# Optimization experiments

Measured on AMD Instinct MI355X. Metric: run time of the kernel, lower is better.

The kernel has to match this reference:

```python
import jax, jax.numpy as jnp
import numpy as np

# Config values (from c.mean_shift / c.cuda in the original module)
EMBED_DIM = 32      # embedding_dim
BW = 2.0            # kernel_bandwidth
ETA = 0.5           # step_size
N_ITERS = 3         # nb_iterations
RES = 96            # pic_res (image is RES x RES, N = RES*RES pixels)


def setup_inputs() -> dict:
    key = jax.random.key(0)
    # Scale 0.1 keeps exp(BW * x^T x) well inside fp32 range, mimicking the
    # bounded embeddings produced by the upstream margin-loss-trained net.
    x_in = 0.1 * jax.random.normal(key, (1, EMBED_DIM, RES, RES), dtype=jnp.float32)
    return {"x_in": x_in}


def reference(x_in):
    # x_in: (1, D, RES, RES). One mean-shift step per iteration:
    #   K = exp(bw * X^T X)                      (N x N affinity)
    #   deg_j = sum_i K[i, j]                    (column degree; K is symmetric)
    #   X_new = eta * X @ (K / deg) + (1-eta) * X
    # (The original's torch.inverse(diag(deg)) is exactly 1/deg column scaling.)
    # All iterates are concatenated along dim 0, as in the torch code.
    res = x_in.shape[3]
    n = res * res
    xs = [x_in.reshape(EMBED_DIM, n)]
    for _ in range(N_ITERS):
        X = xs[-1]                                    # (D, N)
        K = jnp.exp(BW * jnp.einsum('di,dj->ij', X, X))  # (N, N)
        deg = K.sum(axis=0)                           # (N,) column sums
        xs.append(ETA * (X @ (K / deg)) + (1.0 - ETA) * X)
    # (N_ITERS+1, D, RES, RES)
    return jnp.stack(xs, axis=0).reshape(-1, EMBED_DIM, res, res)
```

## Files before the change

### kernel.cpp

```cpp
#include <hip/hip_runtime.h>
#include <hip/hip_bf16.h>


#define DIM 32
#define RESO 96
#define NPT (RESO * RESO)
#define NITER 3
#define ETA 0.5f
#define SCALE 2.88539008f

#define QB 128
#define NQB (NPT / QB)
#define KSEG 7
#define NCHUNK128 (NPT / 128)

typedef __bf16 bf16_t;
typedef __bf16 v8bf __attribute__((ext_vector_type(8)));
typedef float  v4f  __attribute__((ext_vector_type(4)));

__device__ __forceinline__ void gload_lds16(const bf16_t* g, bf16_t* l) {
    __builtin_amdgcn_global_load_lds(
        (const __attribute__((address_space(1))) void*)g,
        (__attribute__((address_space(3))) void*)l, 16, 0, 0);
}

__device__ __forceinline__ int keyinv(int m) {
    return ((m & 8) << 1) | ((m & 4) << 1) | ((m & 16) >> 2) | (m & 3);
}

__global__ __launch_bounds__(256, 4)
void pack_kernel(const float* __restrict__ X,
                 bf16_t* __restrict__ rows,
                 bf16_t* __restrict__ cols,
                 float* __restrict__ out_copy) {
    __shared__ float tt[32][33];
    const int tid = threadIdx.x;
    const int n0  = blockIdx.x * 32;
    const int inv = keyinv(tid & 31);

#pragma unroll
    for (int j = 0; j < 4; ++j) {
        int d = (tid >> 5) + j * 8;
        int n = tid & 31;
        float v = X[(size_t)d * NPT + n0 + n];
        tt[d][n] = v;
        cols[(size_t)d * NPT + n0 + inv] = (bf16_t)v;
        out_copy[(size_t)d * NPT + n0 + n] = v;
    }
    __syncthreads();

#pragma unroll
    for (int j = 0; j < 4; ++j) {
        int n = (tid >> 5) + j * 8;
        int d = tid & 31;
        rows[(size_t)(n0 + n) * DIM + d] = (bf16_t)tt[d][n];
    }
}

__global__ __launch_bounds__(512, 4)
void msattn_kernel(const float* __restrict__ Xcur,
                   const bf16_t* __restrict__ rows,
                   const bf16_t* __restrict__ cols,
                   float* __restrict__ part_num,
                   float* __restrict__ part_den) {
    __shared__ __align__(16) bf16_t tiles[2][8192];

    const int tid  = threadIdx.x;
    const int w    = tid >> 6;
    const int lane = tid & 63;
    const int quad = lane >> 4;
    const int l16  = lane & 15;
    const int qb   = blockIdx.x;
    const int ks   = blockIdx.y;
    const int c0   = (NCHUNK128 * ks) / KSEG;
    const int c1   = (NCHUNK128 * (ks + 1)) / KSEG;
    const int q0w  = qb * QB + w * 16;

    v8bf qfrag;
#pragma unroll
    for (int j = 0; j < 8; ++j) {
        float v = Xcur[(quad * 8 + j) * NPT + q0w + l16];
        qfrag[j] = (bf16_t)(v * SCALE);
    }

    v8bf ones;
#pragma unroll
    for (int j = 0; j < 8; ++j) ones[j] = (bf16_t)1.0f;

    const bf16_t* gsrc;
    int gdelta, hdelta, dstoff;
    if (w < 4) {
        gsrc = rows + ((size_t)c0 * 128 + w * 16 + l16) * DIM + quad * 8;
        gdelta = 128 * DIM;
        hdelta = 64 * DIM;
        dstoff = w * 512;
    } else {
        int r = w - 4, hh = r >> 1, g = r & 1;
        gsrc = cols + (size_t)(hh * 16 + l16) * NPT + c0 * 128 + g * 32 + quad * 8;
        gdelta = 128;
        hdelta = 64;
        dstoff = 2048 + (w - 4) * 512;
    }

    v4f acc0 = {0.f, 0.f, 0.f, 0.f};
    v4f acc1 = {0.f, 0.f, 0.f, 0.f};
    v4f dden = {0.f, 0.f, 0.f, 0.f};

    gload_lds16(gsrc,          &tiles[0][dstoff]);
    gload_lds16(gsrc + hdelta, &tiles[0][4096 + dstoff]);
    gsrc += gdelta;
    __syncthreads();

    for (int c = c0; c < c1; ++c) {
        const int cc = c - c0;
        const bf16_t* tb = tiles[cc & 1];

        if (c + 1 < c1) {
            bf16_t* nt = tiles[(cc + 1) & 1];
            gload_lds16(gsrc,          &nt[dstoff]);
            gload_lds16(gsrc + hdelta, &nt[4096 + dstoff]);
            gsrc += gdelta;
        }

#pragma unroll
        for (int h = 0; h < 2; ++h) {
            const bf16_t* th = tb + h * 4096;

            v4f s[4];
#pragma unroll
            for (int t = 0; t < 4; ++t) {
                v8bf ka = *(const v8bf*)&th[t * 512 + lane * 8];
                s[t] = __builtin_amdgcn_mfma_f32_16x16x32_bf16(ka, qfrag,
                           (v4f){0.f, 0.f, 0.f, 0.f}, 0, 0, 0);
            }

            v8bf b00 = *(const v8bf*)&th[2048 + 0 * 512 + lane * 8];
            v8bf b01 = *(const v8bf*)&th[2048 + 1 * 512 + lane * 8];
            v8bf b10 = *(const v8bf*)&th[2048 + 2 * 512 + lane * 8];
            v8bf b11 = *(const v8bf*)&th[2048 + 3 * 512 + lane * 8];

            v8bf pa0, pa1;
#pragma unroll
            for (int t = 0; t < 2; ++t)
#pragma unroll
                for (int r = 0; r < 4; ++r)
                    pa0[t * 4 + r] = (bf16_t)__builtin_amdgcn_exp2f(s[t][r]);
#pragma unroll
            for (int t = 0; t < 2; ++t)
#pragma unroll
                for (int r = 0; r < 4; ++r)
                    pa1[t * 4 + r] = (bf16_t)__builtin_amdgcn_exp2f(s[2 + t][r]);

            acc0 = __builtin_amdgcn_mfma_f32_16x16x32_bf16(pa0, b00, acc0, 0, 0, 0);
            acc1 = __builtin_amdgcn_mfma_f32_16x16x32_bf16(pa0, b10, acc1, 0, 0, 0);
            dden = __builtin_amdgcn_mfma_f32_16x16x32_bf16(pa0, ones, dden, 0, 0, 0);
            acc0 = __builtin_amdgcn_mfma_f32_16x16x32_bf16(pa1, b01, acc0, 0, 0, 0);
            acc1 = __builtin_amdgcn_mfma_f32_16x16x32_bf16(pa1, b11, acc1, 0, 0, 0);
            dden = __builtin_amdgcn_mfma_f32_16x16x32_bf16(pa1, ones, dden, 0, 0, 0);
        }

        __syncthreads();
    }

    float* pn = part_num + (size_t)ks * NPT * DIM;
#pragma unroll
    for (int r = 0; r < 4; ++r) {
        int gq = q0w + quad * 4 + r;
        pn[(size_t)gq * DIM + l16]      = acc0[r];
        pn[(size_t)gq * DIM + 16 + l16] = acc1[r];
    }
    if (l16 == 0) {
#pragma unroll
        for (int r = 0; r < 4; ++r)
            part_den[ks * NPT + q0w + quad * 4 + r] = dden[r];
    }
}

__global__ __launch_bounds__(512, 2)
void reduce_kernel(const float* __restrict__ part_num,
                   const float* __restrict__ part_den,
                   const float* __restrict__ Xcur,
                   float* __restrict__ Xnext,
                   bf16_t* __restrict__ rows_out,
                   bf16_t* __restrict__ cols_out) {
    __shared__ float tp[2][32][33];
    __shared__ float dpart[KSEG][32];
    __shared__ float txn[32][33];

    const int tid = threadIdx.x;
    const int q0  = blockIdx.x * 32;
    const int inv = keyinv(tid & 31);

    {
        int slot = tid & 255;
        int sh   = tid >> 8;
        int qq = slot >> 3, dq = slot & 7;
        const float* pb = &part_num[(size_t)(q0 + qq) * DIM + dq * 4];
        size_t seg = (size_t)NPT * DIM;
        int ssb = sh * 4;
        v4f s = *(const v4f*)&pb[(ssb + 0) * seg]
              + *(const v4f*)&pb[(ssb + 1) * seg]
              + *(const v4f*)&pb[(ssb + 2) * seg];
        if (sh == 0) s += *(const v4f*)&pb[3 * seg];
#pragma unroll
        for (int k = 0; k < 4; ++k) tp[sh][qq][dq * 4 + k] = s[k];
    }
    if (tid < KSEG * 32) {
        int ss = tid >> 5, q = tid & 31;
        dpart[ss][q] = part_den[ss * NPT + q0 + q];
    }
    __syncthreads();

#pragma unroll
    for (int e = 0; e < 2; ++e) {
        int idx = tid + e * 512;
        int d = idx >> 5, qq = idx & 31;
        float num = tp[0][qq][d] + tp[1][qq][d];
        float dn = dpart[0][qq] + dpart[1][qq] + dpart[2][qq] + dpart[3][qq]
                 + dpart[4][qq] + dpart[5][qq] + dpart[6][qq];
        float xo = Xcur[(size_t)d * NPT + q0 + qq];
        float xn = ETA * num / dn + (1.0f - ETA) * xo;
        Xnext[(size_t)d * NPT + q0 + qq] = xn;
        cols_out[(size_t)d * NPT + q0 + inv] = (bf16_t)xn;
        txn[qq][d] = xn;
    }
    __syncthreads();

#pragma unroll
    for (int e = 0; e < 2; ++e) {
        int idx = tid + e * 512;
        int qq = idx >> 5, d = idx & 31;
        rows_out[(size_t)(q0 + qq) * DIM + d] = (bf16_t)txn[qq][d];
    }
}

extern "C" void kernel_launch(void* const* d_in, const int* in_sizes, int n_in,
                              void* d_out, int out_size, void* d_ws, size_t ws_size,
                              hipStream_t stream) {
    const float* x_in = (const float*)d_in[0];
    float* out = (float*)d_out;

    const size_t DN = (size_t)DIM * NPT;
    bf16_t* rows0 = (bf16_t*)d_ws;
    bf16_t* cols0 = rows0 + DN;
    bf16_t* rows1 = cols0 + DN;
    bf16_t* cols1 = rows1 + DN;
    float* part_num = (float*)(cols1 + DN);
    float* part_den = part_num + (size_t)KSEG * NPT * DIM;

    pack_kernel<<<NPT / 32, 256, 0, stream>>>(x_in, rows0, cols0, out);

    for (int it = 0; it < NITER; ++it) {
        const float* Xcur = (it == 0) ? x_in : out + (size_t)it * DN;
        bf16_t* rin  = (it & 1) ? rows1 : rows0;
        bf16_t* cin  = (it & 1) ? cols1 : cols0;
        bf16_t* rout = (it & 1) ? rows0 : rows1;
        bf16_t* cout = (it & 1) ? cols0 : cols1;
        msattn_kernel<<<dim3(NQB, KSEG), 512, 0, stream>>>(Xcur, rin, cin,
                                                           part_num, part_den);
        reduce_kernel<<<NPT / 32, 512, 0, stream>>>(part_num, part_den, Xcur,
                                                    out + (size_t)(it + 1) * DN,
                                                    rout, cout);
    }
}
```

Before: 123.4 us.

## Keep 144 queries per block in registers and stream keys directly from global

The attention kernel now has each wave hold query fragments for 9 groups of 16 queries (144 per block) in registers. Each wave streams its own slice of keys and values straight from global memory with register double-buffering, replacing the LDS tile pipeline and the per-chunk block barriers. Per-wave partial sums are combined through LDS at the end. The key split drops from 7 to 4 segments, and a pre-scaled bf16 copy of the rows is produced in pack and reduce so the query load needs no conversion. The cost is much higher register pressure (occupancy bound lowered to 2), a cross-wave LDS reduction epilogue, and fewer blocks in the grid (64x4).

```diff
diff --git a/kernel.cpp b/kernel.cpp
--- a/kernel.cpp
+++ b/kernel.cpp
@@ -9,21 +9,17 @@
 #define ETA 0.5f
 #define SCALE 2.88539008f
 
-#define QB 128
+#define QB 144
 #define NQB (NPT / QB)
-#define KSEG 7
-#define NCHUNK128 (NPT / 128)
+#define NG 9
+#define KSEG 4
+#define CHUNK 256
+#define NCHUNK (NPT / CHUNK)
 
 typedef __bf16 bf16_t;
 typedef __bf16 v8bf __attribute__((ext_vector_type(8)));
 typedef float  v4f  __attribute__((ext_vector_type(4)));
 
-__device__ __forceinline__ void gload_lds16(const bf16_t* g, bf16_t* l) {
-    __builtin_amdgcn_global_load_lds(
-        (const __attribute__((address_space(1))) void*)g,
-        (__attribute__((address_space(3))) void*)l, 16, 0, 0);
-}
-
 __device__ __forceinline__ int keyinv(int m) {
     return ((m & 8) << 1) | ((m & 4) << 1) | ((m & 16) >> 2) | (m & 3);
 }
@@ -31,6 +27,7 @@
 __global__ __launch_bounds__(256, 4)
 void pack_kernel(const float* __restrict__ X,
                  bf16_t* __restrict__ rows,
+                 bf16_t* __restrict__ rows_s,
                  bf16_t* __restrict__ cols,
                  float* __restrict__ out_copy) {
     __shared__ float tt[32][33];
@@ -53,17 +50,20 @@
     for (int j = 0; j < 4; ++j) {
         int n = (tid >> 5) + j * 8;
         int d = tid & 31;
-        rows[(size_t)(n0 + n) * DIM + d] = (bf16_t)tt[d][n];
-    }
-}
-
-__global__ __launch_bounds__(512, 4)
-void msattn_kernel(const float* __restrict__ Xcur,
-                   const bf16_t* __restrict__ rows,
+        float v = tt[d][n];
+        rows[(size_t)(n0 + n) * DIM + d]   = (bf16_t)v;
+        rows_s[(size_t)(n0 + n) * DIM + d] = (bf16_t)(v * SCALE);
+    }
+}
+
+__global__ __launch_bounds__(512, 2)
+void msattn_kernel(const bf16_t* __restrict__ rows,
+                   const bf16_t* __restrict__ rows_s,
                    const bf16_t* __restrict__ cols,
                    float* __restrict__ part_num,
                    float* __restrict__ part_den) {
-    __shared__ __align__(16) bf16_t tiles[2][8192];
+    __shared__ float osum[8][48][33];
+    __shared__ float dsum[8][QB];
 
     const int tid  = threadIdx.x;
     const int w    = tid >> 6;
@@ -72,107 +72,105 @@
     const int l16  = lane & 15;
     const int qb   = blockIdx.x;
     const int ks   = blockIdx.y;
-    const int c0   = (NCHUNK128 * ks) / KSEG;
-    const int c1   = (NCHUNK128 * (ks + 1)) / KSEG;
-    const int q0w  = qb * QB + w * 16;
-
-    v8bf qfrag;
-#pragma unroll
-    for (int j = 0; j < 8; ++j) {
-        float v = Xcur[(quad * 8 + j) * NPT + q0w + l16];
-        qfrag[j] = (bf16_t)(v * SCALE);
-    }
+    const int c0   = ks * (NCHUNK / KSEG);
+    const int c1   = c0 + (NCHUNK / KSEG);
+    const int q0   = qb * QB;
+
+    v8bf qf[NG];
+#pragma unroll
+    for (int g = 0; g < NG; ++g)
+        qf[g] = *(const v8bf*)&rows_s[(size_t)(q0 + g * 16 + l16) * DIM + quad * 8];
 
     v8bf ones;
 #pragma unroll
     for (int j = 0; j < 8; ++j) ones[j] = (bf16_t)1.0f;
 
-    const bf16_t* gsrc;
-    int gdelta, hdelta, dstoff;
-    if (w < 4) {
-        gsrc = rows + ((size_t)c0 * 128 + w * 16 + l16) * DIM + quad * 8;
-        gdelta = 128 * DIM;
-        hdelta = 64 * DIM;
-        dstoff = w * 512;
-    } else {
-        int r = w - 4, hh = r >> 1, g = r & 1;
-        gsrc = cols + (size_t)(hh * 16 + l16) * NPT + c0 * 128 + g * 32 + quad * 8;
-        gdelta = 128;
-        hdelta = 64;
-        dstoff = 2048 + (w - 4) * 512;
-    }
-
-    v4f acc0 = {0.f, 0.f, 0.f, 0.f};
-    v4f acc1 = {0.f, 0.f, 0.f, 0.f};
-    v4f dden = {0.f, 0.f, 0.f, 0.f};
-
-    gload_lds16(gsrc,          &tiles[0][dstoff]);
-    gload_lds16(gsrc + hdelta, &tiles[0][4096 + dstoff]);
-    gsrc += gdelta;
-    __syncthreads();
+    const bf16_t* pA = rows + ((size_t)(c0 * CHUNK + w * 32 + l16)) * DIM + quad * 8;
+    const bf16_t* pB = cols + (size_t)l16 * NPT + c0 * CHUNK + w * 32 + quad * 8;
+
+    v4f acc[NG][2];
+    v4f den[NG];
+#pragma unroll
+    for (int g = 0; g < NG; ++g) {
+        acc[g][0] = (v4f){0.f, 0.f, 0.f, 0.f};
+        acc[g][1] = (v4f){0.f, 0.f, 0.f, 0.f};
+        den[g]    = (v4f){0.f, 0.f, 0.f, 0.f};
+    }
+
+    v8bf ka0 = *(const v8bf*)pA;
+    v8bf ka1 = *(const v8bf*)(pA + 16 * DIM);
+    v8bf bV0 = *(const v8bf*)pB;
+    v8bf bV1 = *(const v8bf*)(pB + (size_t)16 * NPT);
+    pA += CHUNK * DIM;
+    pB += CHUNK;
 
     for (int c = c0; c < c1; ++c) {
-        const int cc = c - c0;
-        const bf16_t* tb = tiles[cc & 1];
-
-        if (c + 1 < c1) {
-            bf16_t* nt = tiles[(cc + 1) & 1];
-            gload_lds16(gsrc,          &nt[dstoff]);
-            gload_lds16(gsrc + hdelta, &nt[4096 + dstoff]);
-            gsrc += gdelta;
-        }
-
-#pragma unroll
-        for (int h = 0; h < 2; ++h) {
-            const bf16_t* th = tb + h * 4096;
-
-            v4f s[4];
-#pragma unroll
-            for (int t = 0; t < 4; ++t) {
-                v8bf ka = *(const v8bf*)&th[t * 512 + lane * 8];
-                s[t] = __builtin_amdgcn_mfma_f32_16x16x32_bf16(ka, qfrag,
-                           (v4f){0.f, 0.f, 0.f, 0.f}, 0, 0, 0);
+        const bool more = (c + 1 < c1);
+        v8bf nka0, nka1, nb0, nb1;
+        if (more) {
+            nka0 = *(const v8bf*)pA;
+            nka1 = *(const v8bf*)(pA + 16 * DIM);
+            nb0  = *(const v8bf*)pB;
+            nb1  = *(const v8bf*)(pB + (size_t)16 * NPT);
+            pA += CHUNK * DIM;
+            pB += CHUNK;
+        }
+
+#pragma unroll
+        for (int g = 0; g < NG; ++g) {
+            v4f s0 = __builtin_amdgcn_mfma_f32_16x16x32_bf16(ka0, qf[g],
+                         (v4f){0.f, 0.f, 0.f, 0.f}, 0, 0, 0);
+            v4f s1 = __builtin_amdgcn_mfma_f32_16x16x32_bf16(ka1, qf[g],
+                         (v4f){0.f, 0.f, 0.f, 0.f}, 0, 0, 0);
+            v8bf pa;
+#pragma unroll
+            for (int r = 0; r < 4; ++r) {
+                pa[r]     = (bf16_t)__builtin_amdgcn_exp2f(s0[r]);
+                pa[4 + r] = (bf16_t)__builtin_amdgcn_exp2f(s1[r]);
             }
-
-            v8bf b00 = *(const v8bf*)&th[2048 + 0 * 512 + lane * 8];
-            v8bf b01 = *(const v8bf*)&th[2048 + 1 * 512 + lane * 8];
-            v8bf b10 = *(const v8bf*)&th[2048 + 2 * 512 + lane * 8];
-            v8bf b11 = *(const v8bf*)&th[2048 + 3 * 512 + lane * 8];
-
-            v8bf pa0, pa1;
-#pragma unroll
-            for (int t = 0; t < 2; ++t)
+            acc[g][0] = __builtin_amdgcn_mfma_f32_16x16x32_bf16(pa, bV0, acc[g][0], 0, 0, 0);
+            acc[g][1] = __builtin_amdgcn_mfma_f32_16x16x32_bf16(pa, bV1, acc[g][1], 0, 0, 0);
+            den[g]    = __builtin_amdgcn_mfma_f32_16x16x32_bf16(pa, ones, den[g], 0, 0, 0);
+        }
+
+        if (more) { ka0 = nka0; ka1 = nka1; bV0 = nb0; bV1 = nb1; }
+    }
+
+    if (l16 == 0) {
+#pragma unroll
+        for (int g = 0; g < NG; ++g)
+#pragma unroll
+            for (int r = 0; r < 4; ++r)
+                dsum[w][g * 16 + quad * 4 + r] = den[g][r];
+    }
+
+#pragma unroll
+    for (int round = 0; round < 3; ++round) {
+        if (round) __syncthreads();
+#pragma unroll
+        for (int gg = 0; gg < 3; ++gg) {
+            int g = round * 3 + gg;
+#pragma unroll
+            for (int h = 0; h < 2; ++h)
 #pragma unroll
                 for (int r = 0; r < 4; ++r)
-                    pa0[t * 4 + r] = (bf16_t)__builtin_amdgcn_exp2f(s[t][r]);
-#pragma unroll
-            for (int t = 0; t < 2; ++t)
-#pragma unroll
-                for (int r = 0; r < 4; ++r)
-                    pa1[t * 4 + r] = (bf16_t)__builtin_amdgcn_exp2f(s[2 + t][r]);
-
-            acc0 = __builtin_amdgcn_mfma_f32_16x16x32_bf16(pa0, b00, acc0, 0, 0, 0);
-            acc1 = __builtin_amdgcn_mfma_f32_16x16x32_bf16(pa0, b10, acc1, 0, 0, 0);
-            dden = __builtin_amdgcn_mfma_f32_16x16x32_bf16(pa0, ones, dden, 0, 0, 0);
-            acc0 = __builtin_amdgcn_mfma_f32_16x16x32_bf16(pa1, b01, acc0, 0, 0, 0);
-            acc1 = __builtin_amdgcn_mfma_f32_16x16x32_bf16(pa1, b11, acc1, 0, 0, 0);
-            dden = __builtin_amdgcn_mfma_f32_16x16x32_bf16(pa1, ones, dden, 0, 0, 0);
-        }
-
+                    osum[w][gg * 16 + quad * 4 + r][h * 16 + l16] = acc[g][h][r];
+        }
         __syncthreads();
-    }
-
-    float* pn = part_num + (size_t)ks * NPT * DIM;
-#pragma unroll
-    for (int r = 0; r < 4; ++r) {
-        int gq = q0w + quad * 4 + r;
-        pn[(size_t)gq * DIM + l16]      = acc0[r];
-        pn[(size_t)gq * DIM + 16 + l16] = acc1[r];
-    }
-    if (l16 == 0) {
-#pragma unroll
-        for (int r = 0; r < 4; ++r)
-            part_den[ks * NPT + q0w + quad * 4 + r] = dden[r];
+#pragma unroll
+        for (int e = 0; e < 3; ++e) {
+            int idx = tid + e * 512;
+            int qr = idx >> 5, d = idx & 31;
+            float s = osum[0][qr][d] + osum[1][qr][d] + osum[2][qr][d]
+                    + osum[3][qr][d] + osum[4][qr][d] + osum[5][qr][d]
+                    + osum[6][qr][d] + osum[7][qr][d];
+            part_num[((size_t)ks * NPT + q0 + round * 48 + qr) * DIM + d] = s;
+        }
+    }
+    if (tid < QB) {
+        float s = dsum[0][tid] + dsum[1][tid] + dsum[2][tid] + dsum[3][tid]
+                + dsum[4][tid] + dsum[5][tid] + dsum[6][tid] + dsum[7][tid];
+        part_den[ks * NPT + q0 + tid] = s;
     }
 }
 
@@ -182,6 +180,7 @@
                    const float* __restrict__ Xcur,
                    float* __restrict__ Xnext,
                    bf16_t* __restrict__ rows_out,
+                   bf16_t* __restrict__ rows_s_out,
                    bf16_t* __restrict__ cols_out) {
     __shared__ float tp[2][32][33];
     __shared__ float dpart[KSEG][32];
@@ -197,11 +196,8 @@
         int qq = slot >> 3, dq = slot & 7;
         const float* pb = &part_num[(size_t)(q0 + qq) * DIM + dq * 4];
         size_t seg = (size_t)NPT * DIM;
-        int ssb = sh * 4;
-        v4f s = *(const v4f*)&pb[(ssb + 0) * seg]
-              + *(const v4f*)&pb[(ssb + 1) * seg]
-              + *(const v4f*)&pb[(ssb + 2) * seg];
-        if (sh == 0) s += *(const v4f*)&pb[3 * seg];
+        v4f s = *(const v4f*)&pb[(2 * sh) * seg]
+              + *(const v4f*)&pb[(2 * sh + 1) * seg];
 #pragma unroll
         for (int k = 0; k < 4; ++k) tp[sh][qq][dq * 4 + k] = s[k];
     }
@@ -216,8 +212,7 @@
         int idx = tid + e * 512;
         int d = idx >> 5, qq = idx & 31;
         float num = tp[0][qq][d] + tp[1][qq][d];
-        float dn = dpart[0][qq] + dpart[1][qq] + dpart[2][qq] + dpart[3][qq]
-                 + dpart[4][qq] + dpart[5][qq] + dpart[6][qq];
+        float dn = dpart[0][qq] + dpart[1][qq] + dpart[2][qq] + dpart[3][qq];
         float xo = Xcur[(size_t)d * NPT + q0 + qq];
         float xn = ETA * num / dn + (1.0f - ETA) * xo;
         Xnext[(size_t)d * NPT + q0 + qq] = xn;
@@ -230,7 +225,9 @@
     for (int e = 0; e < 2; ++e) {
         int idx = tid + e * 512;
         int qq = idx >> 5, d = idx & 31;
-        rows_out[(size_t)(q0 + qq) * DIM + d] = (bf16_t)txn[qq][d];
+        float v = txn[qq][d];
+        rows_out[(size_t)(q0 + qq) * DIM + d]   = (bf16_t)v;
+        rows_s_out[(size_t)(q0 + qq) * DIM + d] = (bf16_t)(v * SCALE);
     }
 }
 
@@ -241,25 +238,29 @@
     float* out = (float*)d_out;
 
     const size_t DN = (size_t)DIM * NPT;
-    bf16_t* rows0 = (bf16_t*)d_ws;
-    bf16_t* cols0 = rows0 + DN;
-    bf16_t* rows1 = cols0 + DN;
-    bf16_t* cols1 = rows1 + DN;
+    bf16_t* rows0  = (bf16_t*)d_ws;
+    bf16_t* rowss0 = rows0 + DN;
+    bf16_t* cols0  = rowss0 + DN;
+    bf16_t* rows1  = cols0 + DN;
+    bf16_t* rowss1 = rows1 + DN;
+    bf16_t* cols1  = rowss1 + DN;
     float* part_num = (float*)(cols1 + DN);
     float* part_den = part_num + (size_t)KSEG * NPT * DIM;
 
-    pack_kernel<<<NPT / 32, 256, 0, stream>>>(x_in, rows0, cols0, out);
+    pack_kernel<<<NPT / 32, 256, 0, stream>>>(x_in, rows0, rowss0, cols0, out);
 
     for (int it = 0; it < NITER; ++it) {
         const float* Xcur = (it == 0) ? x_in : out + (size_t)it * DN;
-        bf16_t* rin  = (it & 1) ? rows1 : rows0;
-        bf16_t* cin  = (it & 1) ? cols1 : cols0;
-        bf16_t* rout = (it & 1) ? rows0 : rows1;
-        bf16_t* cout = (it & 1) ? cols0 : cols1;
-        msattn_kernel<<<dim3(NQB, KSEG), 512, 0, stream>>>(Xcur, rin, cin,
+        bf16_t* rin   = (it & 1) ? rows1 : rows0;
+        bf16_t* rsin  = (it & 1) ? rowss1 : rowss0;
+        bf16_t* cin   = (it & 1) ? cols1 : cols0;
+        bf16_t* rout  = (it & 1) ? rows0 : rows1;
+        bf16_t* rsout = (it & 1) ? rowss0 : rowss1;
+        bf16_t* cout  = (it & 1) ? cols0 : cols1;
+        msattn_kernel<<<dim3(NQB, KSEG), 512, 0, stream>>>(rin, rsin, cin,
                                                            part_num, part_den);
         reduce_kernel<<<NPT / 32, 512, 0, stream>>>(part_num, part_den, Xcur,
                                                     out + (size_t)(it + 1) * DN,
-                                                    rout, cout);
-    }
-}
+                                                    rout, rsout, cout);
+    }
+}
```

After: 124.3 us. About the same (+0.8%).
